# Performance work log

Measured on AMD Instinct MI355X. Metric: run time of the kernel, lower is better.

Reference implementation:

```python
import jax, jax.numpy as jnp
import numpy as np

N_NODES = 50000
N_EDGES = 1000000
IN_C, EMB_C, HID_C, EDGE_D = 64, 64, 64, 1
NEG_SLOPE = 0.2


def _seg_softmax(logits, seg, num_segments):
    m = jax.ops.segment_max(logits, seg, num_segments=num_segments)
    e = jnp.exp(logits - m[seg])
    s = jax.ops.segment_sum(e, seg, num_segments=num_segments)
    return e / s[seg]


def _supergat_mx(x, W, att_l, att_r, bias, edge_index, num_nodes):
    # x: [N, Cin], W: [Cin, Cout]; heads=1, concat=False -> output [N, Cout]
    h = x @ W
    loop = jnp.arange(num_nodes)
    src = jnp.concatenate([edge_index[0], loop])  # j (source)
    dst = jnp.concatenate([edge_index[1], loop])  # i (target, softmax group)
    x_j = h[src]  # [E+N, Cout]
    x_i = h[dst]
    logits = jnp.sum(x_i * x_j, axis=-1)  # MX gating
    alpha = jnp.sum(x_j * att_l, axis=-1) + jnp.sum(x_i * att_r, axis=-1)
    alpha = alpha * jax.nn.sigmoid(logits)
    alpha = jax.nn.leaky_relu(alpha, NEG_SLOPE)
    alpha = _seg_softmax(alpha, dst, num_nodes)
    out = jax.ops.segment_sum(x_j * alpha[:, None], dst, num_segments=num_nodes)
    return out + bias


def setup_inputs() -> dict:
    key = jax.random.key(0)
    ks = jax.random.split(key, 16)
    s = 0.05
    inp = {
        "x": jax.random.normal(ks[0], (N_NODES, IN_C), jnp.float32),
        "edge_index": jax.random.randint(ks[1], (2, N_EDGES), 0, N_NODES, jnp.int64),
        "edge_attr": jax.random.normal(ks[2], (N_EDGES, EDGE_D), jnp.float32),
        "W1": jax.random.normal(ks[3], (IN_C, EMB_C), jnp.float32) * s,
        "att_l1": jax.random.normal(ks[4], (EMB_C,), jnp.float32) * s,
        "att_r1": jax.random.normal(ks[5], (EMB_C,), jnp.float32) * s,
        "b1": jnp.zeros((EMB_C,), jnp.float32),
        "W2": jax.random.normal(ks[6], (EMB_C, HID_C), jnp.float32) * s,
        "att_l2": jax.random.normal(ks[7], (HID_C,), jnp.float32) * s,
        "att_r2": jax.random.normal(ks[8], (HID_C,), jnp.float32) * s,
        "b2": jnp.zeros((HID_C,), jnp.float32),
        "Wm1": jax.random.normal(ks[9], (2 * HID_C + EDGE_D, HID_C), jnp.float32) * s,
        "bm1": jnp.zeros((HID_C,), jnp.float32),
        "Wm2": jax.random.normal(ks[10], (HID_C, 1), jnp.float32) * s,
        "bm2": jnp.zeros((1,), jnp.float32),
    }
    return inp


def reference(x, edge_index, edge_attr, W1, att_l1, att_r1, b1,
              W2, att_l2, att_r2, b2, Wm1, bm1, Wm2, bm2):
    n = x.shape[0]
    h = jax.nn.relu(_supergat_mx(x, W1, att_l1, att_r1, b1, edge_index, n))
    h = jax.nn.relu(_supergat_mx(h, W2, att_l2, att_r2, b2, edge_index, n))
    src_h = h[edge_index[0]]
    dst_h = h[edge_index[1]]
    e = jnp.concatenate([src_h, edge_attr, dst_h], axis=-1)  # [E, 2H+edge_dim]
    e = jax.nn.relu(e @ Wm1 + bm1)
    return e @ Wm2 + bm2  # [E, 1]
```

## Files before the change

kernel.cpp:

```cpp
#include <hip/hip_runtime.h>
#include <hip/hip_bf16.h>


#define SCAN_TPB 256
#define SCAN_EPT 8
#define SCAN_CHUNK (SCAN_TPB * SCAN_EPT)
#define NXCD 8
#define GR 16
#define PBLK 512
#define SBLK 32
#define BCAP 250112

__device__ __forceinline__ float alpha_of(float lg, float sl, float sr) {
    float sig = 1.f / (1.f + __expf(-lg));
    float a = (sl + sr) * sig;
    return a > 0.f ? a : 0.2f * a;
}

__device__ __forceinline__ unsigned short f2bf(float f) {
    unsigned u = __float_as_uint(f);
    u += 0x7fffu + ((u >> 16) & 1u);
    return (unsigned short)(u >> 16);
}
__device__ __forceinline__ float bfLO(unsigned u) { return __uint_as_float(u << 16); }
__device__ __forceinline__ float bfHI(unsigned u) { return __uint_as_float(u & 0xffff0000u); }

__global__ __launch_bounds__(256) void gemm64_kernel(
    const float* __restrict__ X, const float* __restrict__ W,
    float* __restrict__ Y, unsigned short* __restrict__ Ybf, int nrows,
    const float* __restrict__ att_l, const float* __restrict__ att_r,
    float* __restrict__ SL, float* __restrict__ SR)
{
    __shared__ float Wl[64 * 64];
    __shared__ float Xs[GR][68];
    int tid = threadIdx.x;
    int base = blockIdx.x * GR;

    {
        const float4* W4 = (const float4*)W;
        float4* Wl4 = (float4*)Wl;
#pragma unroll
        for (int i = 0; i < 4; ++i) Wl4[i * 256 + tid] = W4[i * 256 + tid];
        int r = tid >> 4, q = tid & 15;
        if (base + r < nrows) {
            float4 xv = ((const float4*)X)[(size_t)(base + r) * 16 + q];
            Xs[r][q * 4 + 0] = xv.x; Xs[r][q * 4 + 1] = xv.y;
            Xs[r][q * 4 + 2] = xv.z; Xs[r][q * 4 + 3] = xv.w;
        }
    }
    __syncthreads();

    int r  = tid >> 4;
    int cq = tid & 15;
    int row = base + r;
    if (row >= nrows) return;

    const float4* Wl4 = (const float4*)Wl;
    float4 acc = make_float4(0.f, 0.f, 0.f, 0.f);
#pragma unroll
    for (int k = 0; k < 64; ++k) {
        float xv = Xs[r][k];
        float4 w4 = Wl4[k * 16 + cq];
        acc.x += xv * w4.x; acc.y += xv * w4.y;
        acc.z += xv * w4.z; acc.w += xv * w4.w;
    }
    ((float4*)Y)[(size_t)row * 16 + cq] = acc;
    ushort4 bf;
    bf.x = f2bf(acc.x); bf.y = f2bf(acc.y); bf.z = f2bf(acc.z); bf.w = f2bf(acc.w);
    *(ushort4*)(Ybf + (size_t)row * 64 + cq * 4) = bf;

    if (SL != nullptr) {
        const float4 al = *(const float4*)(att_l + cq * 4);
        const float4 ar = *(const float4*)(att_r + cq * 4);
        float a = acc.x * al.x + acc.y * al.y + acc.z * al.z + acc.w * al.w;
        float b = acc.x * ar.x + acc.y * ar.y + acc.z * ar.z + acc.w * ar.w;
        a += __shfl_xor(a, 1); b += __shfl_xor(b, 1);
        a += __shfl_xor(a, 2); b += __shfl_xor(b, 2);
        a += __shfl_xor(a, 4); b += __shfl_xor(b, 4);
        a += __shfl_xor(a, 8); b += __shfl_xor(b, 8);
        if (cq == 0) { SL[row] = a; SR[row] = b; }
    }
}

__global__ __launch_bounds__(256) void gemm64_dual_kernel(
    const float* __restrict__ X, const float* __restrict__ WA,
    const float* __restrict__ WB,
    unsigned short* __restrict__ Pbf, unsigned short* __restrict__ Qbf,
    int nrows)
{
    __shared__ float Wa[64 * 64];
    __shared__ float Wb[64 * 64];
    __shared__ float Xs[GR][68];
    int tid = threadIdx.x;
    int base = blockIdx.x * GR;

    {
        const float4* A4 = (const float4*)WA;
        const float4* B4 = (const float4*)WB;
        float4* a4 = (float4*)Wa;
        float4* b4 = (float4*)Wb;
#pragma unroll
        for (int i = 0; i < 4; ++i) {
            a4[i * 256 + tid] = A4[i * 256 + tid];
            b4[i * 256 + tid] = B4[i * 256 + tid];
        }
        int r = tid >> 4, q = tid & 15;
        if (base + r < nrows) {
            float4 xv = ((const float4*)X)[(size_t)(base + r) * 16 + q];
            Xs[r][q * 4 + 0] = xv.x; Xs[r][q * 4 + 1] = xv.y;
            Xs[r][q * 4 + 2] = xv.z; Xs[r][q * 4 + 3] = xv.w;
        }
    }
    __syncthreads();

    int r  = tid >> 4;
    int cq = tid & 15;
    int row = base + r;
    if (row >= nrows) return;

    const float4* Wa4 = (const float4*)Wa;
    const float4* Wb4 = (const float4*)Wb;
    float4 accA = make_float4(0.f, 0.f, 0.f, 0.f);
    float4 accB = make_float4(0.f, 0.f, 0.f, 0.f);
#pragma unroll
    for (int k = 0; k < 64; ++k) {
        float xv = Xs[r][k];
        float4 wa = Wa4[k * 16 + cq];
        float4 wb = Wb4[k * 16 + cq];
        accA.x += xv * wa.x; accA.y += xv * wa.y;
        accA.z += xv * wa.z; accA.w += xv * wa.w;
        accB.x += xv * wb.x; accB.y += xv * wb.y;
        accB.z += xv * wb.z; accB.w += xv * wb.w;
    }
    ushort4 pa, qb;
    pa.x = f2bf(accA.x); pa.y = f2bf(accA.y); pa.z = f2bf(accA.z); pa.w = f2bf(accA.w);
    qb.x = f2bf(accB.x); qb.y = f2bf(accB.y); qb.z = f2bf(accB.z); qb.w = f2bf(accB.w);
    *(ushort4*)(Pbf + (size_t)row * 64 + cq * 4) = pa;
    *(ushort4*)(Qbf + (size_t)row * 64 + cq * 4) = qb;
}


__global__ __launch_bounds__(256) void partition_count_kernel(
    const int* __restrict__ src, const int* __restrict__ dst, int E, int N,
    int* __restrict__ bcur, unsigned* __restrict__ buckets)
{
    __shared__ unsigned lbuf[NXCD][512];
    __shared__ int lcnt[NXCD];
    __shared__ int lbase[NXCD];
    int tid = threadIdx.x;
    if (tid < NXCD) lcnt[tid] = 0;
    __syncthreads();

    int chunk = (E + gridDim.x - 1) / gridDim.x;
    int s   = blockIdx.x * chunk;
    int end = s + chunk; if (end > E) end = E;

    for (int base = s; base < end; base += 256) {
        int e = base + tid;
        if (e < end) {
            int ji = dst[e];
            int js = src[e];
            int b = (int)(((long)ji * NXCD) / N);
            if (b > NXCD - 1) b = NXCD - 1;
            int off = ji - (int)(((long)N * b) / NXCD);
            unsigned v = ((unsigned)off << 16) | (unsigned)js;
            int pos = atomicAdd(&lcnt[b], 1);
            lbuf[b][pos] = v;
        }
        __syncthreads();
        if (tid < NXCD) {
            int c = lcnt[tid];
            lbase[tid] = (c >= 256) ? atomicAdd(bcur + tid, 256) : -1;
        }
        __syncthreads();
#pragma unroll
        for (int b = 0; b < NXCD; ++b) {
            int gb = lbase[b];
            if (gb >= 0) {
                int c = lcnt[b];
                unsigned v = lbuf[b][c - 256 + tid];
                buckets[(size_t)b * BCAP + gb + tid] = v;
            }
        }
        __syncthreads();
        if (tid < NXCD && lbase[tid] >= 0) lcnt[tid] -= 256;
        __syncthreads();
    }
    if (tid < NXCD) {
        int c = lcnt[tid];
        lbase[tid] = (c > 0) ? atomicAdd(bcur + tid, c) : -1;
    }
    __syncthreads();
#pragma unroll
    for (int b = 0; b < NXCD; ++b) {
        int c = lcnt[b];
        if (c > 0 && tid < c)
            buckets[(size_t)b * BCAP + lbase[b] + tid] = lbuf[b][tid];
    }
}

__global__ __launch_bounds__(256) void count_bucket_kernel(
    const unsigned* __restrict__ buckets, const int* __restrict__ bcur,
    int* __restrict__ cnt, int N)
{
    int b  = blockIdx.x & (NXCD - 1);
    int sb = blockIdx.x >> 3;
    int sz = bcur[b];
    int lo = (int)(((long)N * b) / NXCD);
    for (int i = sb * 256 + threadIdx.x; i < sz; i += SBLK * 256) {
        unsigned v = buckets[(size_t)b * BCAP + i];
        atomicAdd(cnt + lo + (int)(v >> 16), 1);
    }
}

__global__ __launch_bounds__(SCAN_TPB) void scan_local_kernel(
    const int* __restrict__ cnt, int* __restrict__ starts,
    int* __restrict__ partials, int N)
{
    __shared__ int sh[SCAN_TPB];
    int t = threadIdx.x;
    int base = blockIdx.x * SCAN_CHUNK + t * SCAN_EPT;
    int v[SCAN_EPT];
    int sum = 0;
#pragma unroll
    for (int i = 0; i < SCAN_EPT; ++i) {
        int idx = base + i;
        v[i] = (idx < N) ? cnt[idx] : 0;
        sum += v[i];
    }
    sh[t] = sum;
    __syncthreads();
#pragma unroll
    for (int off = 1; off < SCAN_TPB; off <<= 1) {
        int u = (t >= off) ? sh[t - off] : 0;
        __syncthreads();
        sh[t] += u;
        __syncthreads();
    }
    int run = sh[t] - sum;
#pragma unroll
    for (int i = 0; i < SCAN_EPT; ++i) {
        int idx = base + i;
        if (idx < N) starts[idx] = run;
        run += v[i];
    }
    if (t == SCAN_TPB - 1) partials[blockIdx.x] = sh[SCAN_TPB - 1];
}

__global__ __launch_bounds__(SCAN_TPB) void scan_partials_kernel(
    int* __restrict__ partials, int* __restrict__ starts, int nblk, int N)
{
    __shared__ int sh[SCAN_TPB];
    int t = threadIdx.x;
    int v = (t < nblk) ? partials[t] : 0;
    sh[t] = v;
    __syncthreads();
#pragma unroll
    for (int off = 1; off < SCAN_TPB; off <<= 1) {
        int u = (t >= off) ? sh[t - off] : 0;
        __syncthreads();
        sh[t] += u;
        __syncthreads();
    }
    if (t < nblk) partials[t] = sh[t] - v;
    if (t == SCAN_TPB - 1) starts[N] = sh[SCAN_TPB - 1];
}

__global__ __launch_bounds__(SCAN_TPB) void scan_add_kernel(
    int* __restrict__ starts, int* __restrict__ cursor,
    const int* __restrict__ partials, int N)
{
    int off = partials[blockIdx.x];
    int base = blockIdx.x * SCAN_CHUNK + threadIdx.x * SCAN_EPT;
#pragma unroll
    for (int i = 0; i < SCAN_EPT; ++i) {
        int idx = base + i;
        if (idx < N) {
            int s0 = starts[idx] + off;
            starts[idx] = s0;
            cursor[idx] = s0;
        }
    }
}

__global__ __launch_bounds__(256) void scatter_bucket_kernel(
    const unsigned* __restrict__ buckets, const int* __restrict__ bcur,
    int* __restrict__ cursor, unsigned short* __restrict__ csr16, int N)
{
    int b  = blockIdx.x & (NXCD - 1);
    int sb = blockIdx.x >> 3;
    int sz = bcur[b];
    int lo = (int)(((long)N * b) / NXCD);
    for (int i = sb * 256 + threadIdx.x; i < sz; i += SBLK * 256) {
        unsigned v = buckets[(size_t)b * BCAP + i];
        int node = lo + (int)(v >> 16);
        int p = atomicAdd(cursor + node, 1);
        csr16[p] = (unsigned short)(v & 0xffffu);
    }
}

__global__ __launch_bounds__(256) void node_attn_agg_kernel(
    const float* __restrict__ h, const unsigned short* __restrict__ hbf,
    const unsigned short* __restrict__ csr16, const int* __restrict__ starts,
    const float* __restrict__ SL, const float* __restrict__ SR,
    const float* __restrict__ bias, float* __restrict__ out, int N)
{
    int node = blockIdx.x * 4 + (threadIdx.x >> 6);
    int lane = threadIdx.x & 63;
    int g    = lane >> 3;
    int sub  = lane & 7;
    if (node >= N) return;
    int s = starts[node], t = starts[node + 1];

    const float4 hiA = *(const float4*)(h + (size_t)node * 64 + sub * 8);
    const float4 hiB = *(const float4*)(h + (size_t)node * 64 + sub * 8 + 4);
    float sri = SR[node];

    float c0 = 0.f, c1 = 0.f, c2 = 0.f, c3 = 0.f;
    float c4 = 0.f, c5 = 0.f, c6 = 0.f, c7 = 0.f;
    float ssum = 0.f;

    {
        float lg = hiA.x * hiA.x + hiA.y * hiA.y + hiA.z * hiA.z + hiA.w * hiA.w
                 + hiB.x * hiB.x + hiB.y * hiB.y + hiB.z * hiB.z + hiB.w * hiB.w;
        lg += __shfl_xor(lg, 1);
        lg += __shfl_xor(lg, 2);
        lg += __shfl_xor(lg, 4);
        float a = alpha_of(lg, SL[node], sri);
        float w = __expf(a);
        if (g == 0) {
            ssum = w;
            c0 = w * hiA.x; c1 = w * hiA.y; c2 = w * hiA.z; c3 = w * hiA.w;
            c4 = w * hiB.x; c5 = w * hiB.y; c6 = w * hiB.z; c7 = w * hiB.w;
        }
    }

    for (int k = s + g; k < t; k += 8) {
        int j = csr16[k];
        uint4 hu = *(const uint4*)(hbf + (size_t)j * 64 + sub * 8);
        float h0 = bfLO(hu.x), h1 = bfHI(hu.x), h2 = bfLO(hu.y), h3 = bfHI(hu.y);
        float h4 = bfLO(hu.z), h5 = bfHI(hu.z), h6 = bfLO(hu.w), h7 = bfHI(hu.w);
        float slj = SL[j];
        float lg = hiA.x * h0 + hiA.y * h1 + hiA.z * h2 + hiA.w * h3
                 + hiB.x * h4 + hiB.y * h5 + hiB.z * h6 + hiB.w * h7;
        lg += __shfl_xor(lg, 1);
        lg += __shfl_xor(lg, 2);
        lg += __shfl_xor(lg, 4);
        float a = alpha_of(lg, slj, sri);
        float w = __expf(a);
        ssum += w;
        c0 += w * h0; c1 += w * h1; c2 += w * h2; c3 += w * h3;
        c4 += w * h4; c5 += w * h5; c6 += w * h6; c7 += w * h7;
    }
#pragma unroll
    for (int off = 8; off < 64; off <<= 1) {
        ssum += __shfl_xor(ssum, off);
        c0 += __shfl_xor(c0, off); c1 += __shfl_xor(c1, off);
        c2 += __shfl_xor(c2, off); c3 += __shfl_xor(c3, off);
        c4 += __shfl_xor(c4, off); c5 += __shfl_xor(c5, off);
        c6 += __shfl_xor(c6, off); c7 += __shfl_xor(c7, off);
    }

    if (g == 0) {
        const float4 bA = *(const float4*)(bias + sub * 8);
        const float4 bB = *(const float4*)(bias + sub * 8 + 4);
        float inv = 1.f / ssum;
        float4 vA, vB;
        vA.x = c0 * inv + bA.x; vA.x = vA.x > 0.f ? vA.x : 0.f;
        vA.y = c1 * inv + bA.y; vA.y = vA.y > 0.f ? vA.y : 0.f;
        vA.z = c2 * inv + bA.z; vA.z = vA.z > 0.f ? vA.z : 0.f;
        vA.w = c3 * inv + bA.w; vA.w = vA.w > 0.f ? vA.w : 0.f;
        vB.x = c4 * inv + bB.x; vB.x = vB.x > 0.f ? vB.x : 0.f;
        vB.y = c5 * inv + bB.y; vB.y = vB.y > 0.f ? vB.y : 0.f;
        vB.z = c6 * inv + bB.z; vB.z = vB.z > 0.f ? vB.z : 0.f;
        vB.w = c7 * inv + bB.w; vB.w = vB.w > 0.f ? vB.w : 0.f;
        *(float4*)(out + (size_t)node * 64 + sub * 8)     = vA;
        *(float4*)(out + (size_t)node * 64 + sub * 8 + 4) = vB;
    }
}

__global__ __launch_bounds__(256) void edge_mlp_kernel(
    const unsigned short* __restrict__ Pbf, const unsigned short* __restrict__ Qbf,
    const int* __restrict__ src, const int* __restrict__ dst,
    const float* __restrict__ edge_attr,
    const float* __restrict__ arow, const float* __restrict__ bm1,
    const float* __restrict__ wm2, const float* __restrict__ bm2,
    float* __restrict__ out, int E)
{
    long gid = (long)blockIdx.x * 256 + threadIdx.x;
    int e   = (int)(gid >> 3);
    int sub = (int)(gid & 7);
    if (e >= E) return;
    int js = src[e], ji = dst[e];

    uint4 pu = *(const uint4*)(Pbf + (size_t)js * 64 + sub * 8);
    uint4 qu = *(const uint4*)(Qbf + (size_t)ji * 64 + sub * 8);
    float ea = edge_attr[e];

    const float4 saA = *(const float4*)(arow + sub * 8);
    const float4 saB = *(const float4*)(arow + sub * 8 + 4);
    const float4 swA = *(const float4*)(wm2 + sub * 8);
    const float4 swB = *(const float4*)(wm2 + sub * 8 + 4);
    const float4 bmA = *(const float4*)(bm1 + sub * 8);
    const float4 bmB = *(const float4*)(bm1 + sub * 8 + 4);

    float y, r;
    y = bfLO(pu.x) + bfLO(qu.x) + bmA.x + ea * saA.x; y = y > 0.f ? y : 0.f; r  = y * swA.x;
    y = bfHI(pu.x) + bfHI(qu.x) + bmA.y + ea * saA.y; y = y > 0.f ? y : 0.f; r += y * swA.y;
    y = bfLO(pu.y) + bfLO(qu.y) + bmA.z + ea * saA.z; y = y > 0.f ? y : 0.f; r += y * swA.z;
    y = bfHI(pu.y) + bfHI(qu.y) + bmA.w + ea * saA.w; y = y > 0.f ? y : 0.f; r += y * swA.w;
    y = bfLO(pu.z) + bfLO(qu.z) + bmB.x + ea * saB.x; y = y > 0.f ? y : 0.f; r += y * swB.x;
    y = bfHI(pu.z) + bfHI(qu.z) + bmB.y + ea * saB.y; y = y > 0.f ? y : 0.f; r += y * swB.y;
    y = bfLO(pu.w) + bfLO(qu.w) + bmB.z + ea * saB.z; y = y > 0.f ? y : 0.f; r += y * swB.z;
    y = bfHI(pu.w) + bfHI(qu.w) + bmB.w + ea * saB.w; y = y > 0.f ? y : 0.f; r += y * swB.w;
    r += __shfl_xor(r, 1);
    r += __shfl_xor(r, 2);
    r += __shfl_xor(r, 4);
    if (sub == 0) out[e] = r + bm2[0];
}

extern "C" void kernel_launch(void* const* d_in, const int* in_sizes, int n_in,
                              void* d_out, int out_size, void* d_ws, size_t ws_size,
                              hipStream_t stream)
{
    const float* x     = (const float*)d_in[0];
    const int*   ei    = (const int*)d_in[1];
    const float* eattr = (const float*)d_in[2];
    const float* W1    = (const float*)d_in[3];
    const float* attl1 = (const float*)d_in[4];
    const float* attr1 = (const float*)d_in[5];
    const float* b1    = (const float*)d_in[6];
    const float* W2    = (const float*)d_in[7];
    const float* attl2 = (const float*)d_in[8];
    const float* attr2 = (const float*)d_in[9];
    const float* b2    = (const float*)d_in[10];
    const float* Wm1   = (const float*)d_in[11];
    const float* bm1   = (const float*)d_in[12];
    const float* Wm2   = (const float*)d_in[13];
    const float* bm2   = (const float*)d_in[14];

    int N  = in_sizes[0] / 64;
    int E  = in_sizes[1] / 2;
    const int* srcI = ei;
    const int* dstI = ei + E;

    float* ws       = (float*)d_ws;
    float* hpre     = ws;
    float* h1       = hpre + (size_t)N * 64;
    float* h2       = h1   + (size_t)N * 64;
    float* SL       = h2   + (size_t)N * 64;
    float* SR       = SL + N;
    int*   cnt      = (int*)(SR + N);
    int*   bcur     = cnt + N;
    int*   starts   = bcur + NXCD;
    int*   cursor   = starts + N + 1;
    int*   partials = cursor + N;
    unsigned* buckets = (unsigned*)(partials + SCAN_TPB);
    unsigned short* csr16 = (unsigned short*)(buckets + (size_t)NXCD * BCAP);
    unsigned short* hbf = csr16 + E;
    unsigned short* Pbf = (unsigned short*)hpre;
    unsigned short* Qbf = (unsigned short*)h1;

    dim3 blk(256);
    int gg  = (N + 3) / 4;
    int ggm = (N + GR - 1) / GR;
    int gs  = (N + SCAN_CHUNK - 1) / SCAN_CHUNK;
    int gm  = (int)(((long)E * 8 + 255) / 256);

    hipMemsetAsync(cnt, 0, (size_t)(N + NXCD) * sizeof(int), stream);
    hipLaunchKernelGGL(partition_count_kernel, dim3(PBLK), blk, 0, stream,
                       srcI, dstI, E, N, bcur, buckets);
    hipLaunchKernelGGL(count_bucket_kernel, dim3(NXCD * SBLK), blk, 0, stream,
                       buckets, bcur, cnt, N);
    hipLaunchKernelGGL(scan_local_kernel, dim3(gs), dim3(SCAN_TPB), 0, stream,
                       cnt, starts, partials, N);
    hipLaunchKernelGGL(scan_partials_kernel, dim3(1), dim3(SCAN_TPB), 0, stream,
                       partials, starts, gs, N);
    hipLaunchKernelGGL(scan_add_kernel, dim3(gs), dim3(SCAN_TPB), 0, stream,
                       starts, cursor, partials, N);
    hipLaunchKernelGGL(scatter_bucket_kernel, dim3(NXCD * SBLK), blk, 0, stream,
                       buckets, bcur, cursor, csr16, N);

    hipLaunchKernelGGL(gemm64_kernel, dim3(ggm), blk, 0, stream,
                       x, W1, hpre, hbf, N, attl1, attr1, SL, SR);
    hipLaunchKernelGGL(node_attn_agg_kernel, dim3(gg), blk, 0, stream,
                       hpre, hbf, csr16, starts, SL, SR, b1, h1, N);

    hipLaunchKernelGGL(gemm64_kernel, dim3(ggm), blk, 0, stream,
                       h1, W2, hpre, hbf, N, attl2, attr2, SL, SR);
    hipLaunchKernelGGL(node_attn_agg_kernel, dim3(gg), blk, 0, stream,
                       hpre, hbf, csr16, starts, SL, SR, b2, h2, N);

    hipLaunchKernelGGL(gemm64_dual_kernel, dim3(ggm), blk, 0, stream,
                       h2, Wm1, Wm1 + 65 * 64, Pbf, Qbf, N);
    hipLaunchKernelGGL(edge_mlp_kernel, dim3(gm), blk, 0, stream,
                       Pbf, Qbf, srcI, dstI, eattr,
                       Wm1 + 64 * 64, bm1, Wm2, bm2, (float*)d_out, E);
}
```

Baseline: 367.4 us.

## Fuse degree counting into partition kernel with per-XCD count copies and ballot ranking

Removes the separate count_bucket pass by having the partition kernel atomically increment degree counts directly, into one of eight per-XCD replicated count arrays chosen by block index. The scan then sums the eight copies. LDS slot allocation in the partition kernel now uses wave ballots, with one shared-memory atomic per bucket per wave instead of one per thread. This saves one kernel launch and a re-read of the buckets, at the cost of a larger memset, eight-way reads in the scan, and random global atomics inside the partition loop.

```diff
diff --git a/kernel.cpp b/kernel.cpp
--- a/kernel.cpp
+++ b/kernel.cpp
@@ -142,12 +142,16 @@
 
 __global__ __launch_bounds__(256) void partition_count_kernel(
     const int* __restrict__ src, const int* __restrict__ dst, int E, int N,
-    int* __restrict__ bcur, unsigned* __restrict__ buckets)
+    int* __restrict__ cnt8, int* __restrict__ bcur,
+    unsigned* __restrict__ buckets)
 {
     __shared__ unsigned lbuf[NXCD][512];
     __shared__ int lcnt[NXCD];
     __shared__ int lbase[NXCD];
-    int tid = threadIdx.x;
+    int tid  = threadIdx.x;
+    int lane = tid & 63;
+    int xc   = blockIdx.x & (NXCD - 1);
+    unsigned long long lmask = (1ULL << lane) - 1ULL;
     if (tid < NXCD) lcnt[tid] = 0;
     __syncthreads();
 
@@ -157,16 +161,27 @@
 
     for (int base = s; base < end; base += 256) {
         int e = base + tid;
+        int b = -1; unsigned v = 0;
         if (e < end) {
             int ji = dst[e];
             int js = src[e];
-            int b = (int)(((long)ji * NXCD) / N);
+            b = (int)(((long)ji * NXCD) / N);
             if (b > NXCD - 1) b = NXCD - 1;
             int off = ji - (int)(((long)N * b) / NXCD);
-            unsigned v = ((unsigned)off << 16) | (unsigned)js;
-            int pos = atomicAdd(&lcnt[b], 1);
-            lbuf[b][pos] = v;
-        }
+            v = ((unsigned)off << 16) | (unsigned)js;
+            atomicAdd(cnt8 + (size_t)xc * N + ji, 1);
+        }
+        int rank = 0;
+#pragma unroll
+        for (int bb = 0; bb < NXCD; ++bb) {
+            unsigned long long m = __ballot(b == bb);
+            int cb = __popcll(m);
+            int bs = 0;
+            if (lane == 0 && cb > 0) bs = atomicAdd(&lcnt[bb], cb);
+            bs = __shfl(bs, 0);
+            if (b == bb) rank = bs + __popcll(m & lmask);
+        }
+        if (b >= 0) lbuf[b][rank] = v;
         __syncthreads();
         if (tid < NXCD) {
             int c = lcnt[tid];
@@ -174,12 +189,12 @@
         }
         __syncthreads();
 #pragma unroll
-        for (int b = 0; b < NXCD; ++b) {
-            int gb = lbase[b];
+        for (int bb = 0; bb < NXCD; ++bb) {
+            int gb = lbase[bb];
             if (gb >= 0) {
-                int c = lcnt[b];
-                unsigned v = lbuf[b][c - 256 + tid];
-                buckets[(size_t)b * BCAP + gb + tid] = v;
+                int c = lcnt[bb];
+                unsigned vv = lbuf[bb][c - 256 + tid];
+                buckets[(size_t)bb * BCAP + gb + tid] = vv;
             }
         }
         __syncthreads();
@@ -192,29 +207,15 @@
     }
     __syncthreads();
 #pragma unroll
-    for (int b = 0; b < NXCD; ++b) {
-        int c = lcnt[b];
+    for (int bb = 0; bb < NXCD; ++bb) {
+        int c = lcnt[bb];
         if (c > 0 && tid < c)
-            buckets[(size_t)b * BCAP + lbase[b] + tid] = lbuf[b][tid];
-    }
-}
-
-__global__ __launch_bounds__(256) void count_bucket_kernel(
-    const unsigned* __restrict__ buckets, const int* __restrict__ bcur,
-    int* __restrict__ cnt, int N)
-{
-    int b  = blockIdx.x & (NXCD - 1);
-    int sb = blockIdx.x >> 3;
-    int sz = bcur[b];
-    int lo = (int)(((long)N * b) / NXCD);
-    for (int i = sb * 256 + threadIdx.x; i < sz; i += SBLK * 256) {
-        unsigned v = buckets[(size_t)b * BCAP + i];
-        atomicAdd(cnt + lo + (int)(v >> 16), 1);
+            buckets[(size_t)bb * BCAP + lbase[bb] + tid] = lbuf[bb][tid];
     }
 }
 
 __global__ __launch_bounds__(SCAN_TPB) void scan_local_kernel(
-    const int* __restrict__ cnt, int* __restrict__ starts,
+    const int* __restrict__ cnt8, int* __restrict__ starts,
     int* __restrict__ partials, int N)
 {
     __shared__ int sh[SCAN_TPB];
@@ -225,8 +226,13 @@
 #pragma unroll
     for (int i = 0; i < SCAN_EPT; ++i) {
         int idx = base + i;
-        v[i] = (idx < N) ? cnt[idx] : 0;
-        sum += v[i];
+        int c = 0;
+        if (idx < N) {
+#pragma unroll
+            for (int k = 0; k < NXCD; ++k) c += cnt8[(size_t)k * N + idx];
+        }
+        v[i] = c;
+        sum += c;
     }
     sh[t] = sum;
     __syncthreads();
@@ -450,8 +456,8 @@
     float* h2       = h1   + (size_t)N * 64;
     float* SL       = h2   + (size_t)N * 64;
     float* SR       = SL + N;
-    int*   cnt      = (int*)(SR + N);
-    int*   bcur     = cnt + N;
+    int*   cnt8     = (int*)(SR + N);
+    int*   bcur     = cnt8 + (size_t)NXCD * N;
     int*   starts   = bcur + NXCD;
     int*   cursor   = starts + N + 1;
     int*   partials = cursor + N;
@@ -467,13 +473,11 @@
     int gs  = (N + SCAN_CHUNK - 1) / SCAN_CHUNK;
     int gm  = (int)(((long)E * 8 + 255) / 256);
 
-    hipMemsetAsync(cnt, 0, (size_t)(N + NXCD) * sizeof(int), stream);
+    hipMemsetAsync(cnt8, 0, ((size_t)NXCD * N + NXCD) * sizeof(int), stream);
     hipLaunchKernelGGL(partition_count_kernel, dim3(PBLK), blk, 0, stream,
-                       srcI, dstI, E, N, bcur, buckets);
-    hipLaunchKernelGGL(count_bucket_kernel, dim3(NXCD * SBLK), blk, 0, stream,
-                       buckets, bcur, cnt, N);
+                       srcI, dstI, E, N, cnt8, bcur, buckets);
     hipLaunchKernelGGL(scan_local_kernel, dim3(gs), dim3(SCAN_TPB), 0, stream,
-                       cnt, starts, partials, N);
+                       cnt8, starts, partials, N);
     hipLaunchKernelGGL(scan_partials_kernel, dim3(1), dim3(SCAN_TPB), 0, stream,
                        partials, starts, gs, N);
     hipLaunchKernelGGL(scan_add_kernel, dim3(gs), dim3(SCAN_TPB), 0, stream,
```

New measurement: 362.5 us. Within noise of the previous version (-1.3%).
